# Optimization experiments

Hardware: AMD Instinct MI355X
Metric: run time of the kernel (lower is better)

## Reference

```python
import jax, jax.numpy as jnp
import numpy as np
from jax import lax

V, E, HID, OUT = 32000, 512, 1024, 16000
HD, N, WD = 4, 128, 64          # n_heads, n_words, word_size
T, B = 64, 32
EPS = 1e-6


def oneplus(x):
    return 1.0 + jax.nn.softplus(x)


def setup_inputs() -> dict:
    ks = jax.random.split(jax.random.key(0), 30)
    def w(k, shape, fan_in):
        return jax.random.normal(k, shape, dtype=jnp.float32) * (fan_in ** -0.5)
    lstm_in = E + HD * WD
    return dict(
        src=jax.random.randint(ks[0], (T, B), 0, V),
        emb=jax.random.normal(ks[1], (V, E), dtype=jnp.float32),
        W_ih=w(ks[2], (4 * HID, lstm_in), lstm_in),
        W_hh=w(ks[3], (4 * HID, HID), HID),
        b_ih=w(ks[4], (4 * HID,), HID),
        b_hh=w(ks[5], (4 * HID,), HID),
        rk_w=w(ks[6], (HD, WD, HID), HID), rk_b=w(ks[7], (HD, WD), HID),
        rs_w=w(ks[8], (HD, HID), HID), rs_b=w(ks[9], (HD,), HID),
        fg_w=w(ks[10], (HD, HID), HID), fg_b=w(ks[11], (HD,), HID),
        rm_w=w(ks[12], (HD, 3, HID), HID), rm_b=w(ks[13], (HD, 3), HID),
        wk_w=w(ks[14], (WD, HID), HID), wk_b=w(ks[15], (WD,), HID),
        ws_w=w(ks[16], (1, HID), HID), ws_b=w(ks[17], (1,), HID),
        ev_w=w(ks[18], (WD, HID), HID), ev_b=w(ks[19], (WD,), HID),
        wv_w=w(ks[20], (WD, HID), HID), wv_b=w(ks[21], (WD,), HID),
        ag_w=w(ks[22], (1, HID), HID), ag_b=w(ks[23], (1,), HID),
        wg_w=w(ks[24], (1, HID), HID), wg_b=w(ks[25], (1,), HID),
        Why_w=w(ks[26], (OUT, HID), HID), Why_b=w(ks[27], (OUT,), HID),
        Wry_w=w(ks[28], (OUT, HD * WD), HD * WD),
    )


def _attention(memory, keys, betas):
    # NB: the torch code normalizes `memory` IN PLACE, so the normalized
    # memory replaces the state tensor; we return it to replicate that.
    mem = memory / (jnp.linalg.norm(memory, axis=-1, keepdims=True) + EPS)
    k = keys / jnp.linalg.norm(keys, axis=1, keepdims=True)
    scores = jax.nn.softmax((mem @ k) * betas, axis=1)  # softmax over slots
    return scores, mem


def _forward(src, emb, W_ih, W_hh, b_ih, b_hh, rk_w, rk_b, rs_w, rs_b,
             fg_w, fg_b, rm_w, rm_b, wk_w, wk_b, ws_w, ws_b, ev_w, ev_b,
             wv_w, wv_b, ag_w, ag_b, wg_w, wg_b, Why_w, Why_b, Wry_w):
    Tlen, Bsz = src.shape
    embedded = emb[src]  # [T,B,E]; dropout is identity in eval mode (p=0)
    eye = jnp.eye(N, dtype=emb.dtype)

    def step(carry, e_t):
        h, s, rw, ww, rv, u, p, mem, links = carry
        # rv: [B,WD,HD]; torch reshape(B,-1) is word-major -> row-major here too
        x_t = jnp.concatenate([e_t, rv.reshape(Bsz, -1)], axis=1)
        gates = x_t @ W_ih.T + b_ih + h @ W_hh.T + b_hh
        gi, gf, gg, go = jnp.split(gates, 4, axis=1)
        s = jax.nn.sigmoid(gf) * s + jax.nn.sigmoid(gi) * jnp.tanh(gg)
        h = jax.nn.sigmoid(go) * jnp.tanh(s)
        # per-head interface projections (heads stacked into one einsum)
        free_gates = jax.nn.sigmoid(h @ fg_w.T + fg_b)[:, None, :]          # [B,1,HD]
        read_keys = jnp.einsum('bc,hwc->bwh', h, rk_w) + rk_b.T[None]       # [B,WD,HD]
        read_strengths = oneplus(h @ rs_w.T + rs_b)[:, None, :]             # [B,1,HD]
        read_modes = jax.nn.softmax(jnp.einsum('bc,hmc->bmh', h, rm_w) + rm_b.T[None], axis=1)  # [B,3,HD]
        write_key = h @ wk_w.T + wk_b                                       # [B,WD]
        write_strength = oneplus(h @ ws_w.T + ws_b)                         # [B,1]
        erase = jax.nn.sigmoid(h @ ev_w.T + ev_b)                           # [B,WD]
        writev = jax.nn.sigmoid(h @ wv_w.T + wv_b)                          # [B,WD]
        ag = jax.nn.sigmoid(h @ ag_w.T + ag_b)                              # [B,1]
        wg = jax.nn.sigmoid(h @ wg_w.T + wg_b)                              # [B,1]
        # usage / allocation (note: a stays in sorted order, as in source)
        psi = jnp.exp(jnp.sum(jnp.log(1.0 - free_gates * rw), axis=-1))     # [B,N]
        u = (u + ww - u * ww) * psi
        su = jnp.sort(u, axis=-1)
        a = (1.0 - su) * jnp.exp(jnp.cumsum(jnp.log(su), axis=-1) - jnp.log(su))
        cw, mem = _attention(mem, write_key[..., None], write_strength[..., None])
        ww = wg * (ag * a + (1.0 - ag) * cw[..., 0])                        # [B,N]
        mem = mem + ww[..., None] * (writev - erase)[:, None, :]
        p = (1.0 - ww.sum(axis=1, keepdims=True)) * p + ww
        links = links * (1.0 - (ww[:, :, None] + ww[:, None, :])) + ww[:, :, None] * p[:, None, :]
        links = links * (1.0 - eye)
        cr, mem = _attention(mem, read_keys, read_strengths)                # [B,N,HD]
        f_t = links @ rw
        b_t = jnp.swapaxes(links, 1, 2) @ rw
        rw = (read_modes[:, 0, None, :] * b_t + read_modes[:, 1, None, :] * cr
              + read_modes[:, 2, None, :] * f_t)                           # [B,N,HD]
        rv = jnp.swapaxes(mem, 1, 2) @ rw                                   # [B,WD,HD]
        y = h @ Why_w.T + Why_b + rv.reshape(Bsz, -1) @ Wry_w.T
        return (h, s, rw, ww, rv, u, p, mem, links), y

    z = jnp.zeros
    carry0 = (z((Bsz, HID)), z((Bsz, HID)), z((Bsz, N, HD)), z((Bsz, N)),
              z((Bsz, WD, HD)), jnp.full((Bsz, N), EPS, jnp.float32),
              z((Bsz, N)), z((Bsz, N, WD)), z((Bsz, N, N)))
    _, logits = lax.scan(step, carry0, embedded)
    return logits  # [T,B,OUT]


def reference(src, emb, W_ih, W_hh, b_ih, b_hh, rk_w, rk_b, rs_w, rs_b,
              fg_w, fg_b, rm_w, rm_b, wk_w, wk_b, ws_w, ws_b, ev_w, ev_b,
              wv_w, wv_b, ag_w, ag_b, wg_w, wg_b, Why_w, Why_b, Wry_w):
    return _forward(src, emb, W_ih, W_hh, b_ih, b_hh, rk_w, rk_b, rs_w, rs_b,
                    fg_w, fg_b, rm_w, rm_b, wk_w, wk_b, ws_w, ws_b, ev_w, ev_b,
                    wv_w, wv_b, ag_w, ag_b, wg_w, wg_b, Why_w, Why_b, Wry_w)
```

## Files before the change

### kernel.cpp

```cpp
#include <hip/hip_runtime.h>
#include <math.h>

#define TN 64
#define BN 32
#define EPSF 1e-6f

constexpr long OFF_H     = 0;
constexpr long OFF_RV    = OFF_H    + 65L*32768;
constexpr long OFF_S     = OFF_RV   + 65L*8192;
constexpr long OFF_RW    = OFF_S    + 32768;
constexpr long OFF_WW    = OFF_RW   + 16384;
constexpr long OFF_U     = OFF_WW   + 4096;
constexpr long OFF_P     = OFF_U    + 4096;
constexpr long OFF_MEM   = OFF_P    + 4096;
constexpr long OFF_LINKS = OFF_MEM  + 262144;
constexpr long OFF_PROJ  = OFF_LINKS+ 524288;
constexpr long OFF_SRC   = OFF_PROJ + 16384;
constexpr long OFF_XBF   = OFF_SRC  + 2048;
constexpr long OFF_GW    = OFF_XBF  + 28800;
constexpr long OFF_PW    = OFF_GW   + 3670016;
constexpr long OFF_OW    = OFF_PW   + 245760;
constexpr long WS_NEED   = OFF_OW   + 10240000;

__device__ __forceinline__ float sigm(float x) { return 1.f / (1.f + expf(-x)); }
__device__ __forceinline__ float oneplus_(float x) {
  return 1.f + fmaxf(x, 0.f) + log1pf(expf(-fabsf(x)));
}
__device__ __forceinline__ unsigned short f2bf(float f) {
  unsigned int u = __float_as_uint(f);
  unsigned int r = (u + 0x7FFFu + ((u >> 16) & 1u)) >> 16;
  return (unsigned short)r;
}

typedef __attribute__((ext_vector_type(8))) short bf16x8;
typedef __attribute__((ext_vector_type(4))) float f32x4;

__global__ void src_decode(const void* __restrict__ src_raw, float* __restrict__ ws) {
  __shared__ int is64_s;
  if (threadIdx.x == 0) is64_s = 1;
  __syncthreads();
  const long long* s64 = (const long long*)src_raw;
  for (int i = threadIdx.x; i < 1024; i += 256) {
    long long v = s64[i];
    if (v < 0 || v >= 32000) is64_s = 0;
  }
  __syncthreads();
  int* dst = (int*)(ws + OFF_SRC);
  if (is64_s) {
    for (int i = threadIdx.x; i < 2048; i += 256) dst[i] = (int)s64[i];
  } else {
    const int* s32 = (const int*)src_raw;
    for (int i = threadIdx.x; i < 2048; i += 256) dst[i] = s32[i];
  }
}

__global__ void init_kernel(float* ws, const float* __restrict__ emb) {
  long i0 = (long)blockIdx.x * blockDim.x + threadIdx.x;
  long stride = (long)gridDim.x * blockDim.x;
  for (long x = i0; x < 32768; x += stride) ws[OFF_H + x] = 0.f;
  for (long x = i0; x < 8192;  x += stride) ws[OFF_RV + x] = 0.f;
  const long zlen = OFF_PROJ - OFF_S;
  for (long x = i0; x < zlen; x += stride) {
    long g = OFF_S + x;
    ws[g] = (g >= OFF_U && g < OFF_U + 4096) ? EPSF : 0.f;
  }
  unsigned short* Xg = (unsigned short*)(ws + OFF_XBF);
  const int* src = (const int*)(ws + OFF_SRC);
  for (long x = i0; x < 32 * 1800; x += stride) {
    int b = (int)(x / 1800), k = (int)(x % 1800);
    float v = (k < 512) ? emb[(long)src[b] * 512 + k] : 0.f;
    Xg[x] = f2bf(v);
  }
}

__global__ void wconv_gates(const float* __restrict__ W_ih, const float* __restrict__ W_hh,
                            float* __restrict__ ws) {
  unsigned short* GW = (unsigned short*)(ws + OFF_GW);
  long i0 = (long)blockIdx.x * blockDim.x + threadIdx.x;
  long stride = (long)gridDim.x * blockDim.x;
  const long ngroups = 4096L * 1792 / 4;
  for (long g = i0; g < ngroups; g += stride) {
    long row = g / 448, k = (g % 448) * 4;
    const float* src = (k < 768) ? (W_ih + row * 768 + k) : (W_hh + row * 1024 + (k - 768));
    float4 v = *(const float4*)src;
    unsigned short* d = &GW[row * 1792 + k];
    d[0] = f2bf(v.x); d[1] = f2bf(v.y); d[2] = f2bf(v.z); d[3] = f2bf(v.w);
  }
}

__global__ void wconv_proj(float* __restrict__ ws,
    const float* rk_w, const float* rs_w, const float* fg_w, const float* rm_w,
    const float* wk_w, const float* ws_w, const float* ev_w, const float* wv_w,
    const float* ag_w, const float* wg_w) {
  unsigned short* PW = (unsigned short*)(ws + OFF_PW);
  long i0 = (long)blockIdx.x * blockDim.x + threadIdx.x;
  long stride = (long)gridDim.x * blockDim.x;
  const long ngroups = 471L * 256;
  for (long g = i0; g < ngroups; g += stride) {
    int o = (int)(g / 256), k = (int)(g % 256) * 4;
    const float* w;
    if (o < 256)      { int wi = o >> 2, hh = o & 3; w = rk_w + (long)(hh * 64 + wi) * 1024; }
    else if (o < 260) { w = rs_w + (long)(o - 256) * 1024; }
    else if (o < 264) { w = fg_w + (long)(o - 260) * 1024; }
    else if (o < 276) { int q2 = o - 264, m = q2 >> 2, hh = q2 & 3; w = rm_w + (long)(hh * 3 + m) * 1024; }
    else if (o < 340) { w = wk_w + (long)(o - 276) * 1024; }
    else if (o == 340){ w = ws_w; }
    else if (o < 405) { w = ev_w + (long)(o - 341) * 1024; }
    else if (o < 469) { w = wv_w + (long)(o - 405) * 1024; }
    else if (o == 469){ w = ag_w; }
    else              { w = wg_w; }
    float4 v = *(const float4*)(w + k);
    unsigned short* d = &PW[(long)o * 1024 + k];
    d[0] = f2bf(v.x); d[1] = f2bf(v.y); d[2] = f2bf(v.z); d[3] = f2bf(v.w);
  }
}

__global__ void wconv_out(const float* __restrict__ Why_w, const float* __restrict__ Wry_w,
                          float* __restrict__ ws) {
  unsigned short* OW = (unsigned short*)(ws + OFF_OW);
  long i0 = (long)blockIdx.x * blockDim.x + threadIdx.x;
  long stride = (long)gridDim.x * blockDim.x;
  const long ngroups = 16000L * 1280 / 4;
  for (long g = i0; g < ngroups; g += stride) {
    long row = g / 320, k = (g % 320) * 4;
    const float* src = (k < 1024) ? (Why_w + row * 1024 + k) : (Wry_w + row * 256 + (k - 1024));
    float4 v = *(const float4*)src;
    unsigned short* d = &OW[row * 1280 + k];
    d[0] = f2bf(v.x); d[1] = f2bf(v.y); d[2] = f2bf(v.z); d[3] = f2bf(v.w);
  }
}

constexpr int GSMB = 1024 * 4 + 32 * 1800 * 2;
template <int BF>
__global__ __launch_bounds__(256) void gates_mfma(
    int t, const float* __restrict__ W_ih, const float* __restrict__ W_hh,
    const float* __restrict__ b_ih, const float* __restrict__ b_hh,
    float* __restrict__ ws) {
  extern __shared__ float gsm[];
  float* gle = gsm;
  unsigned short* Xs = (unsigned short*)(gsm + 1024);
  int tid = threadIdx.x;
  int j0 = blockIdx.x * 8;
  {
    const uint4* Xg4 = (const uint4*)(ws + OFF_XBF);
    uint4* Xs4 = (uint4*)Xs;
    for (int i = tid; i < 7200; i += 256) Xs4[i] = Xg4[i];
  }
  __syncthreads();
  int wv = tid >> 6, lane = tid & 63;
  int f = wv & 1, kh = wv >> 1;
  int rsel = lane & 15;
  int kbase = (lane >> 4) * 8 + kh * 896;
  int g = f * 2 + (rsel >> 3);
  int jl = rsel & 7;
  long nrow = (long)g * 1024 + j0 + jl;
  const unsigned short* GW = (const unsigned short*)(ws + OFF_GW);
  f32x4 acc0 = (f32x4){0.f, 0.f, 0.f, 0.f};
  f32x4 acc1 = (f32x4){0.f, 0.f, 0.f, 0.f};
  for (int kt = 0; kt < 28; ++kt) {
    int k = kbase + 32 * kt;
    bf16x8 bfr;
    if (BF) {
      bfr = *(const bf16x8*)&GW[nrow * 1792 + k];
    } else {
      const float* wsrc = (k < 768) ? (W_ih + nrow * 768 + k)
                                    : (W_hh + nrow * 1024 + (k - 768));
      float4 v0 = *(const float4*)(wsrc);
      float4 v1 = *(const float4*)(wsrc + 4);
      bfr[0] = (short)f2bf(v0.x); bfr[1] = (short)f2bf(v0.y);
      bfr[2] = (short)f2bf(v0.z); bfr[3] = (short)f2bf(v0.w);
      bfr[4] = (short)f2bf(v1.x); bfr[5] = (short)f2bf(v1.y);
      bfr[6] = (short)f2bf(v1.z); bfr[7] = (short)f2bf(v1.w);
    }
    bf16x8 a0 = *(const bf16x8*)&Xs[rsel * 1800 + k];
    bf16x8 a1 = *(const bf16x8*)&Xs[(16 + rsel) * 1800 + k];
    acc0 = __builtin_amdgcn_mfma_f32_16x16x32_bf16(a0, bfr, acc0, 0, 0, 0);
    acc1 = __builtin_amdgcn_mfma_f32_16x16x32_bf16(a1, bfr, acc1, 0, 0, 0);
  }
#pragma unroll
  for (int jj = 0; jj < 4; ++jj) {
    int b0 = (lane >> 4) * 4 + jj;
    if (kh == 0) {
      gle[f * 512 + b0 * 16 + rsel] = acc0[jj];
      gle[f * 512 + (b0 + 16) * 16 + rsel] = acc1[jj];
    }
  }
  __syncthreads();
#pragma unroll
  for (int jj = 0; jj < 4; ++jj) {
    int b0 = (lane >> 4) * 4 + jj;
    if (kh == 1) {
      gle[f * 512 + b0 * 16 + rsel] += acc0[jj];
      gle[f * 512 + (b0 + 16) * 16 + rsel] += acc1[jj];
    }
  }
  __syncthreads();
  {
    unsigned short* Xg = (unsigned short*)(ws + OFF_XBF);
    int b = tid >> 3, jle = tid & 7;
    int j = j0 + jle;
    float gi = gle[0 * 512 + b * 16 + jle]     + b_ih[j]        + b_hh[j];
    float gf = gle[0 * 512 + b * 16 + 8 + jle] + b_ih[1024 + j] + b_hh[1024 + j];
    float gg = gle[1 * 512 + b * 16 + jle]     + b_ih[2048 + j] + b_hh[2048 + j];
    float go = gle[1 * 512 + b * 16 + 8 + jle] + b_ih[3072 + j] + b_hh[3072 + j];
    long si = (long)b * 1024 + j;
    float sv = sigm(gf) * ws[OFF_S + si] + sigm(gi) * tanhf(gg);
    ws[OFF_S + si] = sv;
    float hv = sigm(go) * tanhf(sv);
    ws[OFF_H + (long)(t + 1) * 32768 + si] = hv;
    Xg[(long)b * 1800 + 768 + j] = f2bf(hv);
  }
}

template <int BF>
__global__ __launch_bounds__(256) void proj_mfma(
    int t, float* __restrict__ ws,
    const float* rk_w, const float* rk_b, const float* rs_w, const float* rs_b,
    const float* fg_w, const float* fg_b, const float* rm_w, const float* rm_b,
    const float* wk_w, const float* wk_b, const float* ws_w, const float* ws_b,
    const float* ev_w, const float* ev_b, const float* wv_w, const float* wv_b,
    const float* ag_w, const float* ag_b, const float* wg_w, const float* wg_b) {
  __shared__ float pacc[4][512];
  __shared__ float pbias[16];
  int tid = threadIdx.x;
  int wv = tid >> 6, lane = tid & 63;
  int rsel = lane & 15, kofs = (lane >> 4) * 8;
  int o = blockIdx.x * 16 + rsel;
  const float* w;
  float bias;
  int ov = (o < 471) ? o : 470;
  if (ov < 256)      { int wi = ov >> 2, hh = ov & 3; w = rk_w + (long)(hh * 64 + wi) * 1024; bias = rk_b[hh * 64 + wi]; }
  else if (ov < 260) { int q2 = ov - 256; w = rs_w + (long)q2 * 1024; bias = rs_b[q2]; }
  else if (ov < 264) { int q2 = ov - 260; w = fg_w + (long)q2 * 1024; bias = fg_b[q2]; }
  else if (ov < 276) { int q2 = ov - 264, m = q2 >> 2, hh = q2 & 3; w = rm_w + (long)(hh * 3 + m) * 1024; bias = rm_b[hh * 3 + m]; }
  else if (ov < 340) { int q2 = ov - 276; w = wk_w + (long)q2 * 1024; bias = wk_b[q2]; }
  else if (ov == 340){ w = ws_w; bias = ws_b[0]; }
  else if (ov < 405) { int q2 = ov - 341; w = ev_w + (long)q2 * 1024; bias = ev_b[q2]; }
  else if (ov < 469) { int q2 = ov - 405; w = wv_w + (long)q2 * 1024; bias = wv_b[q2]; }
  else if (ov == 469){ w = ag_w; bias = ag_b[0]; }
  else               { w = wg_w; bias = wg_b[0]; }
  if (wv == 0 && lane < 16) pbias[rsel] = bias;
  const unsigned short* Xg = (const unsigned short*)(ws + OFF_XBF);
  const unsigned short* PW = (const unsigned short*)(ws + OFF_PW);
  f32x4 acc0 = (f32x4){0.f, 0.f, 0.f, 0.f};
  f32x4 acc1 = (f32x4){0.f, 0.f, 0.f, 0.f};
#pragma unroll
  for (int kt = 0; kt < 8; ++kt) {
    int k = wv * 256 + kofs + 32 * kt;
    bf16x8 bfr;
    if (BF) {
      bfr = *(const bf16x8*)&PW[(long)ov * 1024 + k];
    } else {
      float4 v0 = *(const float4*)(w + k);
      float4 v1 = *(const float4*)(w + k + 4);
      bfr[0] = (short)f2bf(v0.x); bfr[1] = (short)f2bf(v0.y);
      bfr[2] = (short)f2bf(v0.z); bfr[3] = (short)f2bf(v0.w);
      bfr[4] = (short)f2bf(v1.x); bfr[5] = (short)f2bf(v1.y);
      bfr[6] = (short)f2bf(v1.z); bfr[7] = (short)f2bf(v1.w);
    }
    bf16x8 a0 = *(const bf16x8*)&Xg[(long)rsel * 1800 + 768 + k];
    bf16x8 a1 = *(const bf16x8*)&Xg[(long)(16 + rsel) * 1800 + 768 + k];
    acc0 = __builtin_amdgcn_mfma_f32_16x16x32_bf16(a0, bfr, acc0, 0, 0, 0);
    acc1 = __builtin_amdgcn_mfma_f32_16x16x32_bf16(a1, bfr, acc1, 0, 0, 0);
  }
#pragma unroll
  for (int jj = 0; jj < 4; ++jj) {
    int b0 = (lane >> 4) * 4 + jj;
    pacc[wv][b0 * 16 + rsel] = acc0[jj];
    pacc[wv][(b0 + 16) * 16 + rsel] = acc1[jj];
  }
  __syncthreads();
  for (int idx = tid; idx < 512; idx += 256) {
    int b = idx >> 4, ol = idx & 15;
    int o2 = blockIdx.x * 16 + ol;
    if (o2 < 471) {
      float s = pacc[0][idx] + pacc[1][idx] + pacc[2][idx] + pacc[3][idx];
      ws[OFF_PROJ + (long)b * 512 + o2] = s + pbias[ol];
    }
  }
}

__device__ __forceinline__ float red128_max(float v, float* red, int tid) {
#pragma unroll
  for (int off = 32; off; off >>= 1) v = fmaxf(v, __shfl_xor(v, off));
  if (tid < 128 && (tid & 63) == 0) red[tid >> 6] = v;
  __syncthreads();
  float r = fmaxf(red[0], red[1]);
  __syncthreads();
  return r;
}
__device__ __forceinline__ float red128_sum(float v, float* red, int tid) {
#pragma unroll
  for (int off = 32; off; off >>= 1) v += __shfl_xor(v, off);
  if (tid < 128 && (tid & 63) == 0) red[tid >> 6] = v;
  __syncthreads();
  float r = red[0] + red[1];
  __syncthreads();
  return r;
}

constexpr int SMEMF = 28744;
__global__ __launch_bounds__(256) void memAB_kernel(
    int t, float* __restrict__ ws, const float* __restrict__ emb) {
  extern __shared__ float sm[];
  float* mem_s = sm;
  float* lk_s  = sm + 8320;
  float* red   = sm + 24832;
  float* wwl   = sm + 24840;
  float* pl    = sm + 24968;
  float* kwl   = sm + 25096;
  float* knl   = sm + 25160;
  float* dl    = sm + 25224;
  float* kl    = sm + 25288;
  float* rwold = sm + 25544;
  float* rwnew = sm + 26056;
  float* fpart = sm + 26568;
  float* bpart = sm + 27592;
  float* su    = sm + 28616;
  int b = blockIdx.x, tid = threadIdx.x;
  int n = tid & 127, half = tid >> 7, lane = tid & 63;
  const float* pj = ws + OFF_PROJ + b * 512;
  float* u    = ws + OFF_U  + b * 128;
  float* wwp  = ws + OFF_WW + b * 128;
  float* pp   = ws + OFF_P  + b * 128;
  float* rwp  = ws + OFF_RW + b * 512;
  float* memp = ws + OFF_MEM + (long)b * 8192;
  float* lk   = ws + OFF_LINKS + (long)b * 16384;

  for (int i = tid; i < 8192; i += 256) mem_s[(i >> 6) * 65 + (i & 63)] = memp[i];
  for (int i = tid; i < 16384; i += 256) lk_s[(i >> 7) * 129 + (i & 127)] = lk[i];

  float uu = 0.f;
  if (half == 0) {
    float fg0 = sigm(pj[260]), fg1 = sigm(pj[261]), fg2 = sigm(pj[262]), fg3 = sigm(pj[263]);
    float r0 = rwp[n * 4], r1 = rwp[n * 4 + 1], r2 = rwp[n * 4 + 2], r3 = rwp[n * 4 + 3];
    rwold[n * 4] = r0; rwold[n * 4 + 1] = r1; rwold[n * 4 + 2] = r2; rwold[n * 4 + 3] = r3;
    float psi = expf(logf(1.f - fg0 * r0) + logf(1.f - fg1 * r1) +
                     logf(1.f - fg2 * r2) + logf(1.f - fg3 * r3));
    float u0 = u[n], wwo = wwp[n];
    uu = (u0 + wwo - u0 * wwo) * psi;
    u[n] = uu;
  }
  if (tid < 64) {
    kwl[tid] = pj[276 + tid];
    dl[tid] = sigm(pj[405 + tid]) - sigm(pj[341 + tid]);
  }
  if (tid >= 128 && tid < 192) {
    int q = tid - 128;
#pragma unroll
    for (int h = 0; h < 4; ++h) kl[q * 4 + h] = pj[q * 4 + h];
  }
  __syncthreads();
  float kn2 = 0.f;
#pragma unroll
  for (int w = 0; w < 64; ++w) kn2 += kwl[w] * kwl[w];
  float kn = sqrtf(kn2);
  if (tid < 64) knl[tid] = kwl[tid] / kn;

  float v = uu;
  if (half == 0) {
#pragma unroll
    for (int k = 2; k <= 64; k <<= 1) {
#pragma unroll
      for (int j = k >> 1; j > 0; j >>= 1) {
        float other = __shfl_xor(v, j);
        bool up = ((n & k) == 0);
        bool high = (n & j) != 0;
        float mn = fminf(v, other), mx2 = fmaxf(v, other);
        v = (high == up) ? mx2 : mn;
      }
    }
    su[n] = v;
  }
  __syncthreads();
  if (half == 0) {
    float other = su[n ^ 64];
    v = ((n & 64) != 0) ? fmaxf(v, other) : fminf(v, other);
#pragma unroll
    for (int j = 32; j > 0; j >>= 1) {
      float other2 = __shfl_xor(v, j);
      bool high = (n & j) != 0;
      v = high ? fmaxf(v, other2) : fminf(v, other2);
    }
  }
  float lgv = 0.f;
  if (half == 0) {
    lgv = logf(v);
#pragma unroll
    for (int d = 1; d < 64; d <<= 1) {
      float t2 = __shfl_up(lgv, d);
      lgv = (lane >= d) ? lgv + t2 : lgv;
    }
  }
  if (tid == 63) red[0] = lgv;
  __syncthreads();
  if (half == 0 && (tid >> 6) == 1) lgv += red[0];
  __syncthreads();
  float mrow[64];
  float score = -3.4e38f, e = 0.f, wwn = 0.f, a_n = 0.f;
  if (half == 0) {
    a_n = (1.f - v) * expf(lgv - logf(v));
    float sq = 0.f;
#pragma unroll
    for (int w = 0; w < 64; ++w) { float m = mem_s[n * 65 + w]; mrow[w] = m; sq += m * m; }
    float den = sqrtf(sq) + EPSF;
#pragma unroll
    for (int w = 0; w < 64; ++w) mrow[w] = mrow[w] / den;
    float dot = 0.f;
#pragma unroll
    for (int w = 0; w < 64; ++w) dot += mrow[w] * knl[w];
    score = dot * oneplus_(pj[340]);
  }
  float mx = red128_max(score, red, tid);
  e = (half == 0) ? expf(score - mx) : 0.f;
  float esum = red128_sum(e, red, tid);
  if (half == 0) {
    float cw = e / esum;
    float ag = sigm(pj[469]), wg = sigm(pj[470]);
    wwn = wg * (ag * a_n + (1.f - ag) * cw);
    wwp[n] = wwn; wwl[n] = wwn;
  }
  float sumww = red128_sum((half == 0) ? wwn : 0.f, red, tid);
  if (half == 0) {
    float pn = (1.f - sumww) * pp[n] + wwn;
    pp[n] = pn; pl[n] = pn;
  }
  __syncthreads();
  if (half == 0) {
#pragma unroll
    for (int w = 0; w < 64; ++w) mem_s[n * 65 + w] = mrow[w] + wwn * dl[w];
  }
  {
    float wn = wwl[n], pcol = pl[n];
    int base = half * 64;
    for (int q = 0; q < 64; ++q) {
      int k2 = base + q;
      float lv = lk_s[k2 * 129 + n] * (1.f - (wwl[k2] + wn)) + wwl[k2] * pcol;
      lk_s[k2 * 129 + n] = (k2 == n) ? 0.f : lv;
    }
  }
  __syncthreads();

  if (half == 0) {
    float sq = 0.f;
#pragma unroll
    for (int w = 0; w < 64; ++w) { float m = mem_s[n * 65 + w]; mrow[w] = m; sq += m * m; }
    float den2 = sqrtf(sq) + EPSF;
#pragma unroll
    for (int w = 0; w < 64; ++w) { mrow[w] = mrow[w] / den2; mem_s[n * 65 + w] = mrow[w]; }
  }
  __syncthreads();
  float cr_[4];
#pragma unroll
  for (int h = 0; h < 4; ++h) {
    float s3 = 0.f;
#pragma unroll
    for (int w = 0; w < 64; ++w) { float kv = kl[w * 4 + h]; s3 += kv * kv; }
    float knh = sqrtf(s3);
    float sc = -3.4e38f;
    if (half == 0) {
      float d2 = 0.f;
#pragma unroll
      for (int w = 0; w < 64; ++w) d2 += mrow[w] * (kl[w * 4 + h] / knh);
      sc = d2 * oneplus_(pj[256 + h]);
    }
    float mxh = red128_max(sc, red, tid);
    float eh = (half == 0) ? expf(sc - mxh) : 0.f;
    float ehs = red128_sum(eh, red, tid);
    cr_[h] = eh / ehs;
  }
  {
    float f0 = 0, f1 = 0, f2 = 0, f3 = 0, b0 = 0, b1 = 0, b2 = 0, b3 = 0;
    int base = half * 64;
    for (int q = 0; q < 64; ++q) {
      int jj = base + q;
      float lrow = lk_s[n * 129 + jj];
      float lcol = lk_s[jj * 129 + n];
      float q0 = rwold[jj * 4], q1 = rwold[jj * 4 + 1], q2 = rwold[jj * 4 + 2], q3 = rwold[jj * 4 + 3];
      f0 += lrow * q0; f1 += lrow * q1; f2 += lrow * q2; f3 += lrow * q3;
      b0 += lcol * q0; b1 += lcol * q1; b2 += lcol * q2; b3 += lcol * q3;
    }
    int o = half * 512 + n * 4;
    fpart[o] = f0; fpart[o + 1] = f1; fpart[o + 2] = f2; fpart[o + 3] = f3;
    bpart[o] = b0; bpart[o + 1] = b1; bpart[o + 2] = b2; bpart[o + 3] = b3;
  }
  __syncthreads();
  if (half == 0) {
#pragma unroll
    for (int h = 0; h < 4; ++h) {
      float fv = fpart[n * 4 + h] + fpart[512 + n * 4 + h];
      float bv = bpart[n * 4 + h] + bpart[512 + n * 4 + h];
      float m0 = pj[264 + h], m1 = pj[264 + 4 + h], m2 = pj[264 + 8 + h];
      float mm = fmaxf(m0, fmaxf(m1, m2));
      float e0 = expf(m0 - mm), e1 = expf(m1 - mm), e2 = expf(m2 - mm);
      float inv = 1.f / (e0 + e1 + e2);
      float rwv = (e0 * inv) * bv + (e1 * inv) * cr_[h] + (e2 * inv) * fv;
      rwp[n * 4 + h] = rwv;
      rwnew[n * 4 + h] = rwv;
    }
  }
  __syncthreads();
  for (int i = tid; i < 8192; i += 256) memp[i] = mem_s[(i >> 6) * 65 + (i & 63)];
  for (int i = tid; i < 16384; i += 256) lk[i] = lk_s[(i >> 7) * 129 + (i & 127)];
  unsigned short* Xg = (unsigned short*)(ws + OFF_XBF);
  {
    int w2 = tid & 63, which = tid >> 6;
    float rv = 0.f;
    for (int jj = 0; jj < 128; ++jj) rv += mem_s[jj * 65 + w2] * rwnew[jj * 4 + which];
    ws[OFF_RV + (long)(t + 1) * 8192 + b * 256 + w2 * 4 + which] = rv;
    Xg[(long)b * 1800 + 512 + w2 * 4 + which] = f2bf(rv);
  }
  if (t + 1 < TN) {
    int nsrc = ((const int*)(ws + OFF_SRC))[(t + 1) * 32 + b];
    const float* eb = emb + (long)nsrc * 512;
    for (int i = tid; i < 512; i += 256) Xg[(long)b * 1800 + i] = f2bf(eb[i]);
  }
}

template <int BF>
__global__ __launch_bounds__(512) void out_gemm_mfma(
    const float* __restrict__ ws, const float* __restrict__ Why_w,
    const float* __restrict__ Why_b, const float* __restrict__ Wry_w,
    float* __restrict__ out) {
  __shared__ unsigned short As[256 * 40];
  __shared__ unsigned short Bs[128 * 40];
  const float* Hp  = ws + OFF_H + 32768;
  const float* RVp = ws + OFF_RV + 8192;
  const unsigned short* OW = (const unsigned short*)(ws + OFF_OW);
  int tid = threadIdx.x;
  int wv = tid >> 6, lane = tid & 63;
  int wr = wv >> 1, wc = wv & 1;
  int col0 = blockIdx.x * 128, row0 = blockIdx.y * 256;
  f32x4 acc[4][4];
#pragma unroll
  for (int i = 0; i < 4; ++i)
#pragma unroll
    for (int j = 0; j < 4; ++j) acc[i][j] = (f32x4){0.f, 0.f, 0.f, 0.f};

  for (int kt = 0; kt < 40; ++kt) {
    int k0 = kt * 32;
    __syncthreads();
    {
      int r = tid >> 1, kh = tid & 1;
      int gk = k0 + kh * 16;
      long grow = row0 + r;
      const float* src = (gk < 1024) ? (Hp + grow * 1024 + gk)
                                     : (RVp + grow * 256 + (gk - 1024));
      float4 v0 = *(const float4*)(src);
      float4 v1 = *(const float4*)(src + 4);
      float4 v2 = *(const float4*)(src + 8);
      float4 v3 = *(const float4*)(src + 12);
      unsigned short* d = &As[r * 40 + kh * 16];
      d[0] = f2bf(v0.x);  d[1] = f2bf(v0.y);  d[2] = f2bf(v0.z);  d[3] = f2bf(v0.w);
      d[4] = f2bf(v1.x);  d[5] = f2bf(v1.y);  d[6] = f2bf(v1.z);  d[7] = f2bf(v1.w);
      d[8] = f2bf(v2.x);  d[9] = f2bf(v2.y);  d[10] = f2bf(v2.z); d[11] = f2bf(v2.w);
      d[12] = f2bf(v3.x); d[13] = f2bf(v3.y); d[14] = f2bf(v3.z); d[15] = f2bf(v3.w);
    }
    {
      int r = tid >> 2, ks = (tid & 3) * 8;
      int gk = k0 + ks;
      long wrow = col0 + r;
      if (BF) {
        *(uint4*)&Bs[r * 40 + ks] = *(const uint4*)&OW[wrow * 1280 + gk];
      } else {
        const float* src = (gk < 1024) ? (Why_w + wrow * 1024 + gk)
                                       : (Wry_w + wrow * 256 + (gk - 1024));
        float4 v0 = *(const float4*)(src);
        float4 v1 = *(const float4*)(src + 4);
        unsigned short* d = &Bs[r * 40 + ks];
        d[0] = f2bf(v0.x); d[1] = f2bf(v0.y); d[2] = f2bf(v0.z); d[3] = f2bf(v0.w);
        d[4] = f2bf(v1.x); d[5] = f2bf(v1.y); d[6] = f2bf(v1.z); d[7] = f2bf(v1.w);
      }
    }
    __syncthreads();
    bf16x8 afr[4], bfr[4];
    int kofs = (lane >> 4) * 8;
    int rsel = lane & 15;
#pragma unroll
    for (int mt = 0; mt < 4; ++mt)
      afr[mt] = *(const bf16x8*)&As[(wr * 64 + mt * 16 + rsel) * 40 + kofs];
#pragma unroll
    for (int nt = 0; nt < 4; ++nt)
      bfr[nt] = *(const bf16x8*)&Bs[(wc * 64 + nt * 16 + rsel) * 40 + kofs];
#pragma unroll
    for (int mt = 0; mt < 4; ++mt)
#pragma unroll
      for (int nt = 0; nt < 4; ++nt)
        acc[mt][nt] = __builtin_amdgcn_mfma_f32_16x16x32_bf16(afr[mt], bfr[nt], acc[mt][nt], 0, 0, 0);
  }
  int crow = (lane >> 4) * 4, ccol = lane & 15;
#pragma unroll
  for (int nt = 0; nt < 4; ++nt) {
    int gcol = col0 + wc * 64 + nt * 16 + ccol;
    float bias = Why_b[gcol];
#pragma unroll
    for (int mt = 0; mt < 4; ++mt) {
      long grow = row0 + wr * 64 + mt * 16 + crow;
#pragma unroll
      for (int j = 0; j < 4; ++j) {
        out[(grow + j) * 16000 + gcol] = acc[mt][nt][j] + bias;
      }
    }
  }
}

extern "C" void kernel_launch(void* const* d_in, const int* in_sizes, int n_in,
                              void* d_out, int out_size, void* d_ws, size_t ws_size,
                              hipStream_t stream) {
  const void* src_raw = d_in[0];
  const float* emb   = (const float*)d_in[1];
  const float* W_ih  = (const float*)d_in[2];
  const float* W_hh  = (const float*)d_in[3];
  const float* b_ih  = (const float*)d_in[4];
  const float* b_hh  = (const float*)d_in[5];
  const float* rk_w  = (const float*)d_in[6];
  const float* rk_b  = (const float*)d_in[7];
  const float* rs_w  = (const float*)d_in[8];
  const float* rs_b  = (const float*)d_in[9];
  const float* fg_w  = (const float*)d_in[10];
  const float* fg_b  = (const float*)d_in[11];
  const float* rm_w  = (const float*)d_in[12];
  const float* rm_b  = (const float*)d_in[13];
  const float* wk_w  = (const float*)d_in[14];
  const float* wk_b  = (const float*)d_in[15];
  const float* ws_w  = (const float*)d_in[16];
  const float* ws_b  = (const float*)d_in[17];
  const float* ev_w  = (const float*)d_in[18];
  const float* ev_b  = (const float*)d_in[19];
  const float* wv_w  = (const float*)d_in[20];
  const float* wv_b  = (const float*)d_in[21];
  const float* ag_w  = (const float*)d_in[22];
  const float* ag_b  = (const float*)d_in[23];
  const float* wg_w  = (const float*)d_in[24];
  const float* wg_b  = (const float*)d_in[25];
  const float* Why_w = (const float*)d_in[26];
  const float* Why_b = (const float*)d_in[27];
  const float* Wry_w = (const float*)d_in[28];
  float* ws = (float*)d_ws;
  float* out = (float*)d_out;

  const bool big = (ws_size >= (size_t)WS_NEED * sizeof(float));
  src_decode<<<1, 256, 0, stream>>>(src_raw, ws);
  init_kernel<<<512, 256, 0, stream>>>(ws, emb);
  if (big) {
    wconv_gates<<<1024, 256, 0, stream>>>(W_ih, W_hh, ws);
    wconv_proj<<<471, 256, 0, stream>>>(ws, rk_w, rs_w, fg_w, rm_w, wk_w, ws_w,
                                        ev_w, wv_w, ag_w, wg_w);
    wconv_out<<<2048, 256, 0, stream>>>(Why_w, Wry_w, ws);
  }
  const size_t smem_bytes = (size_t)SMEMF * sizeof(float);
  for (int t = 0; t < TN; ++t) {
    if (big) gates_mfma<1><<<128, 256, GSMB, stream>>>(t, W_ih, W_hh, b_ih, b_hh, ws);
    else     gates_mfma<0><<<128, 256, GSMB, stream>>>(t, W_ih, W_hh, b_ih, b_hh, ws);
    if (big) proj_mfma<1><<<30, 256, 0, stream>>>(t, ws, rk_w, rk_b, rs_w, rs_b, fg_w, fg_b,
                                                  rm_w, rm_b, wk_w, wk_b, ws_w, ws_b,
                                                  ev_w, ev_b, wv_w, wv_b, ag_w, ag_b, wg_w, wg_b);
    else     proj_mfma<0><<<30, 256, 0, stream>>>(t, ws, rk_w, rk_b, rs_w, rs_b, fg_w, fg_b,
                                                  rm_w, rm_b, wk_w, wk_b, ws_w, ws_b,
                                                  ev_w, ev_b, wv_w, wv_b, ag_w, ag_b, wg_w, wg_b);
    memAB_kernel<<<32, 256, smem_bytes, stream>>>(t, ws, emb);
  }
  if (big) out_gemm_mfma<1><<<dim3(125, 8), 512, 0, stream>>>(ws, Why_w, Why_b, Wry_w, out);
  else     out_gemm_mfma<0><<<dim3(125, 8), 512, 0, stream>>>(ws, Why_w, Why_b, Wry_w, out);
}
```

Measured before the change: 3.678 ms.

## Fuse controller projection into memory kernel, split gates K over four waves

```diff
diff --git a/kernel.cpp b/kernel.cpp
--- a/kernel.cpp
+++ b/kernel.cpp
@@ -20,7 +20,11 @@
 constexpr long OFF_GW    = OFF_XBF  + 28800;
 constexpr long OFF_PW    = OFF_GW   + 3670016;
 constexpr long OFF_OW    = OFF_PW   + 245760;
-constexpr long WS_NEED   = OFF_OW   + 10240000;
+constexpr long WS_NEED1  = OFF_OW   + 10240000;
+constexpr long OFF_HBF   = WS_NEED1;
+constexpr long OFF_RVBF  = OFF_HBF  + 1064960;
+constexpr long OFF_PB    = OFF_RVBF + 266240;
+constexpr long WS_NEED2  = OFF_PB   + 480;
 
 __device__ __forceinline__ float sigm(float x) { return 1.f / (1.f + expf(-x)); }
 __device__ __forceinline__ float oneplus_(float x) {
@@ -88,10 +92,13 @@
   }
 }
 
-__global__ void wconv_proj(float* __restrict__ ws,
+__global__ void wconv_proj(float* __restrict__ ws, int fill_pb,
     const float* rk_w, const float* rs_w, const float* fg_w, const float* rm_w,
     const float* wk_w, const float* ws_w, const float* ev_w, const float* wv_w,
-    const float* ag_w, const float* wg_w) {
+    const float* ag_w, const float* wg_w,
+    const float* rk_b, const float* rs_b, const float* fg_b, const float* rm_b,
+    const float* wk_b, const float* ws_b, const float* ev_b, const float* wv_b,
+    const float* ag_b, const float* wg_b) {
   unsigned short* PW = (unsigned short*)(ws + OFF_PW);
   long i0 = (long)blockIdx.x * blockDim.x + threadIdx.x;
   long stride = (long)gridDim.x * blockDim.x;
@@ -113,6 +120,23 @@
     unsigned short* d = &PW[(long)o * 1024 + k];
     d[0] = f2bf(v.x); d[1] = f2bf(v.y); d[2] = f2bf(v.z); d[3] = f2bf(v.w);
   }
+  if (fill_pb) {
+    float* PB = ws + OFF_PB;
+    for (long o = i0; o < 471; o += stride) {
+      float bias;
+      if (o < 256)      { int wi = (int)o >> 2, hh = (int)o & 3; bias = rk_b[hh * 64 + wi]; }
+      else if (o < 260) { bias = rs_b[o - 256]; }
+      else if (o < 264) { bias = fg_b[o - 260]; }
+      else if (o < 276) { long q2 = o - 264, m = q2 >> 2, hh = q2 & 3; bias = rm_b[hh * 3 + m]; }
+      else if (o < 340) { bias = wk_b[o - 276]; }
+      else if (o == 340){ bias = ws_b[0]; }
+      else if (o < 405) { bias = ev_b[o - 341]; }
+      else if (o < 469) { bias = wv_b[o - 405]; }
+      else if (o == 469){ bias = ag_b[0]; }
+      else              { bias = wg_b[0]; }
+      PB[o] = bias;
+    }
+  }
 }
 
 __global__ void wconv_out(const float* __restrict__ Why_w, const float* __restrict__ Wry_w,
@@ -130,17 +154,17 @@
   }
 }
 
-constexpr int GSMB = 1024 * 4 + 32 * 1800 * 2;
-template <int BF>
+constexpr int GSMF = 2048 + 28800;
+template <int BF, int HBW>
 __global__ __launch_bounds__(256) void gates_mfma(
     int t, const float* __restrict__ W_ih, const float* __restrict__ W_hh,
     const float* __restrict__ b_ih, const float* __restrict__ b_hh,
     float* __restrict__ ws) {
   extern __shared__ float gsm[];
   float* gle = gsm;
-  unsigned short* Xs = (unsigned short*)(gsm + 1024);
+  unsigned short* Xs = (unsigned short*)(gsm + 2048);
   int tid = threadIdx.x;
-  int j0 = blockIdx.x * 8;
+  int j0 = blockIdx.x * 4;
   {
     const uint4* Xg4 = (const uint4*)(ws + OFF_XBF);
     uint4* Xs4 = (uint4*)Xs;
@@ -148,16 +172,16 @@
   }
   __syncthreads();
   int wv = tid >> 6, lane = tid & 63;
-  int f = wv & 1, kh = wv >> 1;
+  int kh = wv;
   int rsel = lane & 15;
-  int kbase = (lane >> 4) * 8 + kh * 896;
-  int g = f * 2 + (rsel >> 3);
-  int jl = rsel & 7;
+  int kbase = (lane >> 4) * 8 + kh * 448;
+  int g = rsel >> 2;
+  int jl = rsel & 3;
   long nrow = (long)g * 1024 + j0 + jl;
   const unsigned short* GW = (const unsigned short*)(ws + OFF_GW);
   f32x4 acc0 = (f32x4){0.f, 0.f, 0.f, 0.f};
   f32x4 acc1 = (f32x4){0.f, 0.f, 0.f, 0.f};
-  for (int kt = 0; kt < 28; ++kt) {
+  for (int kt = 0; kt < 14; ++kt) {
     int k = kbase + 32 * kt;
     bf16x8 bfr;
     if (BF) {
@@ -180,35 +204,37 @@
 #pragma unroll
   for (int jj = 0; jj < 4; ++jj) {
     int b0 = (lane >> 4) * 4 + jj;
-    if (kh == 0) {
-      gle[f * 512 + b0 * 16 + rsel] = acc0[jj];
-      gle[f * 512 + (b0 + 16) * 16 + rsel] = acc1[jj];
-    }
-  }
-  __syncthreads();
-#pragma unroll
-  for (int jj = 0; jj < 4; ++jj) {
-    int b0 = (lane >> 4) * 4 + jj;
-    if (kh == 1) {
-      gle[f * 512 + b0 * 16 + rsel] += acc0[jj];
-      gle[f * 512 + (b0 + 16) * 16 + rsel] += acc1[jj];
-    }
-  }
-  __syncthreads();
-  {
+    gle[wv * 512 + b0 * 16 + rsel] = acc0[jj];
+    gle[wv * 512 + (b0 + 16) * 16 + rsel] = acc1[jj];
+  }
+  __syncthreads();
+  if (tid < 128) {
     unsigned short* Xg = (unsigned short*)(ws + OFF_XBF);
-    int b = tid >> 3, jle = tid & 7;
+    int b = tid >> 2, jle = tid & 3;
     int j = j0 + jle;
-    float gi = gle[0 * 512 + b * 16 + jle]     + b_ih[j]        + b_hh[j];
-    float gf = gle[0 * 512 + b * 16 + 8 + jle] + b_ih[1024 + j] + b_hh[1024 + j];
-    float gg = gle[1 * 512 + b * 16 + jle]     + b_ih[2048 + j] + b_hh[2048 + j];
-    float go = gle[1 * 512 + b * 16 + 8 + jle] + b_ih[3072 + j] + b_hh[3072 + j];
+    float gi = gle[0 * 512 + b * 16 + jle]      + gle[1 * 512 + b * 16 + jle]
+             + gle[2 * 512 + b * 16 + jle]      + gle[3 * 512 + b * 16 + jle]
+             + b_ih[j] + b_hh[j];
+    float gf = gle[0 * 512 + b * 16 + 4 + jle]  + gle[1 * 512 + b * 16 + 4 + jle]
+             + gle[2 * 512 + b * 16 + 4 + jle]  + gle[3 * 512 + b * 16 + 4 + jle]
+             + b_ih[1024 + j] + b_hh[1024 + j];
+    float gg = gle[0 * 512 + b * 16 + 8 + jle]  + gle[1 * 512 + b * 16 + 8 + jle]
+             + gle[2 * 512 + b * 16 + 8 + jle]  + gle[3 * 512 + b * 16 + 8 + jle]
+             + b_ih[2048 + j] + b_hh[2048 + j];
+    float go = gle[0 * 512 + b * 16 + 12 + jle] + gle[1 * 512 + b * 16 + 12 + jle]
+             + gle[2 * 512 + b * 16 + 12 + jle] + gle[3 * 512 + b * 16 + 12 + jle]
+             + b_ih[3072 + j] + b_hh[3072 + j];
     long si = (long)b * 1024 + j;
     float sv = sigm(gf) * ws[OFF_S + si] + sigm(gi) * tanhf(gg);
     ws[OFF_S + si] = sv;
     float hv = sigm(go) * tanhf(sv);
     ws[OFF_H + (long)(t + 1) * 32768 + si] = hv;
-    Xg[(long)b * 1800 + 768 + j] = f2bf(hv);
+    unsigned short hb = f2bf(hv);
+    Xg[(long)b * 1800 + 768 + j] = hb;
+    if (HBW) {
+      unsigned short* HB = (unsigned short*)(ws + OFF_HBF);
+      HB[(long)(t + 1) * 32768 + si] = hb;
+    }
   }
 }
 
@@ -299,7 +325,9 @@
   return r;
 }
 
-constexpr int SMEMF = 28744;
+constexpr int SMEMF  = 28744;
+constexpr int SMEMF2 = 28744 + 512 + 1024;
+template <int FUSE, int RBW>
 __global__ __launch_bounds__(256) void memAB_kernel(
     int t, float* __restrict__ ws, const float* __restrict__ emb) {
   extern __shared__ float sm[];
@@ -317,15 +345,44 @@
   float* fpart = sm + 26568;
   float* bpart = sm + 27592;
   float* su    = sm + 28616;
+  float* pjl   = sm + 28744;
+  float* hsh   = sm + 29256;
   int b = blockIdx.x, tid = threadIdx.x;
   int n = tid & 127, half = tid >> 7, lane = tid & 63;
-  const float* pj = ws + OFF_PROJ + b * 512;
   float* u    = ws + OFF_U  + b * 128;
   float* wwp  = ws + OFF_WW + b * 128;
   float* pp   = ws + OFF_P  + b * 128;
   float* rwp  = ws + OFF_RW + b * 512;
   float* memp = ws + OFF_MEM + (long)b * 8192;
   float* lk   = ws + OFF_LINKS + (long)b * 16384;
+
+  if (FUSE) {
+    const unsigned short* Xgb = (const unsigned short*)(ws + OFF_XBF) + (long)b * 1800 + 768;
+    for (int i = tid; i < 1024; i += 256)
+      hsh[i] = __uint_as_float(((unsigned int)Xgb[i]) << 16);
+    __syncthreads();
+    const unsigned short* PW = (const unsigned short*)(ws + OFF_PW);
+    const float* PB = ws + OFF_PB;
+    for (int o = tid; o < 471; o += 256) {
+      const uint4* wr4 = (const uint4*)&PW[(long)o * 1024];
+      float s = 0.f;
+      for (int kq = 0; kq < 128; ++kq) {
+        uint4 wv4 = wr4[kq];
+        int k = kq * 8;
+        s += __uint_as_float((wv4.x & 0xFFFFu) << 16) * hsh[k];
+        s += __uint_as_float(wv4.x & 0xFFFF0000u)     * hsh[k + 1];
+        s += __uint_as_float((wv4.y & 0xFFFFu) << 16) * hsh[k + 2];
+        s += __uint_as_float(wv4.y & 0xFFFF0000u)     * hsh[k + 3];
+        s += __uint_as_float((wv4.z & 0xFFFFu) << 16) * hsh[k + 4];
+        s += __uint_as_float(wv4.z & 0xFFFF0000u)     * hsh[k + 5];
+        s += __uint_as_float((wv4.w & 0xFFFFu) << 16) * hsh[k + 6];
+        s += __uint_as_float(wv4.w & 0xFFFF0000u)     * hsh[k + 7];
+      }
+      pjl[o] = s + PB[o];
+    }
+    __syncthreads();
+  }
+  const float* pj = FUSE ? pjl : (ws + OFF_PROJ + b * 512);
 
   for (int i = tid; i < 8192; i += 256) mem_s[(i >> 6) * 65 + (i & 63)] = memp[i];
   for (int i = tid; i < 16384; i += 256) lk_s[(i >> 7) * 129 + (i & 127)] = lk[i];
@@ -508,7 +565,12 @@
     float rv = 0.f;
     for (int jj = 0; jj < 128; ++jj) rv += mem_s[jj * 65 + w2] * rwnew[jj * 4 + which];
     ws[OFF_RV + (long)(t + 1) * 8192 + b * 256 + w2 * 4 + which] = rv;
-    Xg[(long)b * 1800 + 512 + w2 * 4 + which] = f2bf(rv);
+    unsigned short rb = f2bf(rv);
+    Xg[(long)b * 1800 + 512 + w2 * 4 + which] = rb;
+    if (RBW) {
+      unsigned short* RB = (unsigned short*)(ws + OFF_RVBF);
+      RB[(long)(t + 1) * 8192 + b * 256 + w2 * 4 + which] = rb;
+    }
   }
   if (t + 1 < TN) {
     int nsrc = ((const int*)(ws + OFF_SRC))[(t + 1) * 32 + b];
@@ -517,7 +579,7 @@
   }
 }
 
-template <int BF>
+template <int BF, int ABF>
 __global__ __launch_bounds__(512) void out_gemm_mfma(
     const float* __restrict__ ws, const float* __restrict__ Why_w,
     const float* __restrict__ Why_b, const float* __restrict__ Wry_w,
@@ -527,6 +589,8 @@
   const float* Hp  = ws + OFF_H + 32768;
   const float* RVp = ws + OFF_RV + 8192;
   const unsigned short* OW = (const unsigned short*)(ws + OFF_OW);
+  const unsigned short* HB16 = (const unsigned short*)(ws + OFF_HBF) + 32768;
+  const unsigned short* RB16 = (const unsigned short*)(ws + OFF_RVBF) + 8192;
   int tid = threadIdx.x;
   int wv = tid >> 6, lane = tid & 63;
   int wr = wv >> 1, wc = wv & 1;
@@ -544,17 +608,27 @@
       int r = tid >> 1, kh = tid & 1;
       int gk = k0 + kh * 16;
       long grow = row0 + r;
-      const float* src = (gk < 1024) ? (Hp + grow * 1024 + gk)
-                                     : (RVp + grow * 256 + (gk - 1024));
-      float4 v0 = *(const float4*)(src);
-      float4 v1 = *(const float4*)(src + 4);
-      float4 v2 = *(const float4*)(src + 8);
-      float4 v3 = *(const float4*)(src + 12);
-      unsigned short* d = &As[r * 40 + kh * 16];
-      d[0] = f2bf(v0.x);  d[1] = f2bf(v0.y);  d[2] = f2bf(v0.z);  d[3] = f2bf(v0.w);
-      d[4] = f2bf(v1.x);  d[5] = f2bf(v1.y);  d[6] = f2bf(v1.z);  d[7] = f2bf(v1.w);
-      d[8] = f2bf(v2.x);  d[9] = f2bf(v2.y);  d[10] = f2bf(v2.z); d[11] = f2bf(v2.w);
-      d[12] = f2bf(v3.x); d[13] = f2bf(v3.y); d[14] = f2bf(v3.z); d[15] = f2bf(v3.w);
+      if (ABF) {
+        const unsigned short* srcb = (gk < 1024) ? (HB16 + grow * 1024 + gk)
+                                                 : (RB16 + grow * 256 + (gk - 1024));
+        uint4 p0 = *(const uint4*)(srcb);
+        uint4 p1 = *(const uint4*)(srcb + 8);
+        unsigned short* d = &As[r * 40 + kh * 16];
+        *(uint4*)d = p0;
+        *(uint4*)(d + 8) = p1;
+      } else {
+        const float* src = (gk < 1024) ? (Hp + grow * 1024 + gk)
+                                       : (RVp + grow * 256 + (gk - 1024));
+        float4 v0 = *(const float4*)(src);
+        float4 v1 = *(const float4*)(src + 4);
+        float4 v2 = *(const float4*)(src + 8);
+        float4 v3 = *(const float4*)(src + 12);
+        unsigned short* d = &As[r * 40 + kh * 16];
+        d[0] = f2bf(v0.x);  d[1] = f2bf(v0.y);  d[2] = f2bf(v0.z);  d[3] = f2bf(v0.w);
+        d[4] = f2bf(v1.x);  d[5] = f2bf(v1.y);  d[6] = f2bf(v1.z);  d[7] = f2bf(v1.w);
+        d[8] = f2bf(v2.x);  d[9] = f2bf(v2.y);  d[10] = f2bf(v2.z); d[11] = f2bf(v2.w);
+        d[12] = f2bf(v3.x); d[13] = f2bf(v3.y); d[14] = f2bf(v3.z); d[15] = f2bf(v3.w);
+      }
     }
     {
       int r = tid >> 2, ks = (tid & 3) * 8;
@@ -639,27 +713,36 @@
   float* ws = (float*)d_ws;
   float* out = (float*)d_out;
 
-  const bool big = (ws_size >= (size_t)WS_NEED * sizeof(float));
+  const bool t2 = (ws_size >= (size_t)WS_NEED2 * sizeof(float));
+  const bool t1 = !t2 && (ws_size >= (size_t)WS_NEED1 * sizeof(float));
   src_decode<<<1, 256, 0, stream>>>(src_raw, ws);
   init_kernel<<<512, 256, 0, stream>>>(ws, emb);
-  if (big) {
+  if (t1 || t2) {
     wconv_gates<<<1024, 256, 0, stream>>>(W_ih, W_hh, ws);
-    wconv_proj<<<471, 256, 0, stream>>>(ws, rk_w, rs_w, fg_w, rm_w, wk_w, ws_w,
-                                        ev_w, wv_w, ag_w, wg_w);
+    wconv_proj<<<471, 256, 0, stream>>>(ws, t2 ? 1 : 0,
+                                        rk_w, rs_w, fg_w, rm_w, wk_w, ws_w,
+                                        ev_w, wv_w, ag_w, wg_w,
+                                        rk_b, rs_b, fg_b, rm_b, wk_b, ws_b,
+                                        ev_b, wv_b, ag_b, wg_b);
     wconv_out<<<2048, 256, 0, stream>>>(Why_w, Wry_w, ws);
   }
-  const size_t smem_bytes = (size_t)SMEMF * sizeof(float);
+  const size_t gsm_bytes = (size_t)GSMF * sizeof(float);
   for (int t = 0; t < TN; ++t) {
-    if (big) gates_mfma<1><<<128, 256, GSMB, stream>>>(t, W_ih, W_hh, b_ih, b_hh, ws);
-    else     gates_mfma<0><<<128, 256, GSMB, stream>>>(t, W_ih, W_hh, b_ih, b_hh, ws);
-    if (big) proj_mfma<1><<<30, 256, 0, stream>>>(t, ws, rk_w, rk_b, rs_w, rs_b, fg_w, fg_b,
-                                                  rm_w, rm_b, wk_w, wk_b, ws_w, ws_b,
-                                                  ev_w, ev_b, wv_w, wv_b, ag_w, ag_b, wg_w, wg_b);
-    else     proj_mfma<0><<<30, 256, 0, stream>>>(t, ws, rk_w, rk_b, rs_w, rs_b, fg_w, fg_b,
-                                                  rm_w, rm_b, wk_w, wk_b, ws_w, ws_b,
-                                                  ev_w, ev_b, wv_w, wv_b, ag_w, ag_b, wg_w, wg_b);
-    memAB_kernel<<<32, 256, smem_bytes, stream>>>(t, ws, emb);
-  }
-  if (big) out_gemm_mfma<1><<<dim3(125, 8), 512, 0, stream>>>(ws, Why_w, Why_b, Wry_w, out);
-  else     out_gemm_mfma<0><<<dim3(125, 8), 512, 0, stream>>>(ws, Why_w, Why_b, Wry_w, out);
-}
+    if (t2)      gates_mfma<1, 1><<<256, 256, gsm_bytes, stream>>>(t, W_ih, W_hh, b_ih, b_hh, ws);
+    else if (t1) gates_mfma<1, 0><<<256, 256, gsm_bytes, stream>>>(t, W_ih, W_hh, b_ih, b_hh, ws);
+    else         gates_mfma<0, 0><<<256, 256, gsm_bytes, stream>>>(t, W_ih, W_hh, b_ih, b_hh, ws);
+    if (!t2) {
+      if (t1) proj_mfma<1><<<30, 256, 0, stream>>>(t, ws, rk_w, rk_b, rs_w, rs_b, fg_w, fg_b,
+                                                   rm_w, rm_b, wk_w, wk_b, ws_w, ws_b,
+                                                   ev_w, ev_b, wv_w, wv_b, ag_w, ag_b, wg_w, wg_b);
+      else    proj_mfma<0><<<30, 256, 0, stream>>>(t, ws, rk_w, rk_b, rs_w, rs_b, fg_w, fg_b,
+                                                   rm_w, rm_b, wk_w, wk_b, ws_w, ws_b,
+                                                   ev_w, ev_b, wv_w, wv_b, ag_w, ag_b, wg_w, wg_b);
+    }
+    if (t2) memAB_kernel<1, 1><<<32, 256, (size_t)SMEMF2 * sizeof(float), stream>>>(t, ws, emb);
+    else    memAB_kernel<0, 0><<<32, 256, (size_t)SMEMF * sizeof(float), stream>>>(t, ws, emb);
+  }
+  if (t2)      out_gemm_mfma<1, 1><<<dim3(125, 8), 512, 0, stream>>>(ws, Why_w, Why_b, Wry_w, out);
+  else if (t1) out_gemm_mfma<1, 0><<<dim3(125, 8), 512, 0, stream>>>(ws, Why_w, Why_b, Wry_w, out);
+  else         out_gemm_mfma<0, 0><<<dim3(125, 8), 512, 0, stream>>>(ws, Why_w, Why_b, Wry_w, out);
+}
```

New measurement: 5.535 ms. 1.5x slower.
